# Kernel tuning notes

Hardware: AMD Instinct MI355X
Metric: run time of the kernel (lower is better)

## Reference

```python
import jax, jax.numpy as jnp
import numpy as np

B, T, F, H = 1024, 100, 64, 256


def _unif(key, shape, stdv):
    return jax.random.uniform(key, shape, jnp.float32, -stdv, stdv)


def setup_inputs() -> dict:
    key = jax.random.key(0)
    ks = jax.random.split(key, 20)
    X = jax.random.normal(ks[0], (B, T, F), jnp.float32)
    missing_mask = jnp.round(jax.random.uniform(ks[1], (B, T, F), jnp.float32))
    deltas = jax.random.uniform(ks[2], (B, T, F), jnp.float32)
    s_h = 1.0 / np.sqrt(H)
    s_f = 1.0 / np.sqrt(F)
    return {
        "X": X, "missing_mask": missing_mask, "deltas": deltas,
        # TemporalDecay h: W [H,F], b [H] (stdv = 1/sqrt(out=H))
        "W_dh": _unif(ks[3], (H, F), s_h), "b_dh": _unif(ks[4], (H,), s_h),
        # TemporalDecay x (diag): W [F,F], b [F]
        "W_dx": _unif(ks[5], (F, F), s_f), "b_dx": _unif(ks[6], (F,), s_f),
        # hist_reg: Linear(H -> F)
        "W_hist": _unif(ks[7], (F, H), s_h), "b_hist": _unif(ks[8], (F,), s_h),
        # feat_reg: W [F,F] masked by (1 - I), b [F]
        "W_feat": _unif(ks[9], (F, F), s_f), "b_feat": _unif(ks[10], (F,), s_f),
        # weight_combine: Linear(2F -> F)
        "W_comb": _unif(ks[11], (F, 2 * F), 1.0 / np.sqrt(2 * F)),
        "b_comb": _unif(ks[12], (F,), 1.0 / np.sqrt(2 * F)),
        # LSTMCell(2F -> H): gates order i,f,g,o
        "W_ih": _unif(ks[13], (4 * H, 2 * F), s_h), "b_ih": _unif(ks[14], (4 * H,), s_h),
        "W_hh": _unif(ks[15], (4 * H, H), s_h), "b_hh": _unif(ks[16], (4 * H,), s_h),
    }


def _masked_mae(inp, tgt, mask):
    return jnp.sum(jnp.abs(inp - tgt) * mask) / (jnp.sum(mask) + 1e-9)


def _rits(X, missing_mask, deltas, W_dh, b_dh, W_dx, b_dx, W_hist, b_hist,
          W_feat, b_feat, W_comb, b_comb, W_ih, b_ih, W_hh, b_hh):
    f = X.shape[-1]
    w_dx_diag = jnp.diag(W_dx)                       # diag TemporalDecay: W * eye
    W_feat_m = W_feat * (1.0 - jnp.eye(f, dtype=W_feat.dtype))

    def step(carry, xt):
        h, c, rec_loss, rec_mae = carry
        x, m, d = xt                                  # each [B, F]
        gamma_h = jnp.exp(-jax.nn.relu(d @ W_dh.T + b_dh))   # [B, H]
        gamma_x = jnp.exp(-jax.nn.relu(d * w_dx_diag + b_dx))  # [B, F]
        h = h * gamma_h
        x_h = h @ W_hist.T + b_hist
        rec_loss = rec_loss + _masked_mae(x_h, x, m)
        x_c = m * x + (1.0 - m) * x_h
        z_h = x_c @ W_feat_m.T + b_feat
        rec_loss = rec_loss + _masked_mae(z_h, x, m)
        alpha = jax.nn.sigmoid(jnp.concatenate([gamma_x, m], axis=1) @ W_comb.T + b_comb)
        c_h = alpha * z_h + (1.0 - alpha) * x_h
        rec_mae = rec_mae + _masked_mae(c_h, x, m)
        rec_loss = rec_loss + rec_mae                 # faithful to source (cumulative MAE added)
        c_c = m * x + (1.0 - m) * c_h
        inputs = jnp.concatenate([c_c, m], axis=1)    # [B, 2F]
        gates = inputs @ W_ih.T + b_ih + h @ W_hh.T + b_hh
        i_g, f_g, g_g, o_g = jnp.split(gates, 4, axis=1)
        c = jax.nn.sigmoid(f_g) * c + jax.nn.sigmoid(i_g) * jnp.tanh(g_g)
        h = jax.nn.sigmoid(o_g) * jnp.tanh(c)
        return (h, c, rec_loss, rec_mae), c_h

    b = X.shape[0]
    hsz = W_hh.shape[1]
    init = (jnp.zeros((b, hsz), X.dtype), jnp.zeros((b, hsz), X.dtype),
            jnp.asarray(0.0, X.dtype), jnp.asarray(0.0, X.dtype))
    xs = (jnp.swapaxes(X, 0, 1), jnp.swapaxes(missing_mask, 0, 1), jnp.swapaxes(deltas, 0, 1))
    (h, c, rec_loss, rec_mae), ests = jax.lax.scan(step, init, xs)
    estimations = jnp.swapaxes(ests, 0, 1)            # [B, T, F]
    imputed = missing_mask * X + (1.0 - missing_mask) * estimations
    seq_len = X.shape[1]
    return imputed, rec_mae / seq_len, rec_loss / (seq_len * 3)


def reference(X, missing_mask, deltas, W_dh, b_dh, W_dx, b_dx, W_hist, b_hist,
              W_feat, b_feat, W_comb, b_comb, W_ih, b_ih, W_hh, b_hh):
    return _rits(X, missing_mask, deltas, W_dh, b_dh, W_dx, b_dx, W_hist, b_hist,
                 W_feat, b_feat, W_comb, b_comb, W_ih, b_ih, W_hh, b_hh)
```

## Files before the change

kernel.cpp:

```cpp
#include <hip/hip_runtime.h>
#include <hip/hip_bf16.h>


#define Bz 1024
#define Tz 100
#define Fz 64
#define Hz 256
#define GROUPS 64
#define SIBS 4
#define RPB 16

typedef __attribute__((ext_vector_type(8))) short short8;
typedef __attribute__((ext_vector_type(4))) float floatx4;
typedef __hip_bfloat16 bf16;
typedef unsigned long long u64;

#define MFMA16(a, b, c) __builtin_amdgcn_mfma_f32_16x16x32_bf16((a), (b), (c), 0, 0, 0)

__device__ __forceinline__ float sigmf(float x) { return 1.0f / (1.0f + __expf(-x)); }
__device__ __forceinline__ float tanhfast(float x) { return 2.0f / (1.0f + __expf(-2.0f * x)) - 1.0f; }


__global__ void rits_convert(const float* __restrict__ Wdh, const float* __restrict__ Wdx,
                             const float* __restrict__ Whist, const float* __restrict__ Wfeat,
                             const float* __restrict__ Wcomb, const float* __restrict__ Wih,
                             const float* __restrict__ Whh, bf16* __restrict__ wsbf,
                             float* __restrict__ wdxd, unsigned int* __restrict__ flagsArr) {
    int idx = blockIdx.x * blockDim.x + threadIdx.x;
    if (idx < 4096) flagsArr[idx] = 0u;
    if (idx < 64) wdxd[idx] = Wdx[idx * 65];
    if (idx >= 438272) return;
    float v;
    if (idx < 16384) v = Wdh[idx];
    else if (idx < 32768) v = Whist[idx - 16384];
    else if (idx < 36864) { int i = idx - 32768; v = ((i >> 6) == (i & 63)) ? 0.0f : Wfeat[i]; }
    else if (idx < 45056) v = Wcomb[idx - 36864];
    else {
        int i = idx - 45056;
        int e = i & 7, q = (i >> 3) & 3, l = (i >> 5) & 15, g = (i >> 9) & 3, w = (i >> 11) & 15;
        int s = i >> 15;
        int n = g * 256 + w * 16 + l;
        v = (s < 4) ? Wih[n * 128 + s * 32 + q * 8 + e] : Whh[n * 256 + (s - 4) * 32 + q * 8 + e];
    }
    wsbf[idx] = __float2bfloat16(v);
}

__global__ __launch_bounds__(1024, 4) void rits_main(
    const float* __restrict__ X, const float* __restrict__ Mm, const float* __restrict__ Dd,
    const float* __restrict__ b_dh, const float* __restrict__ b_dx,
    const float* __restrict__ b_hist, const float* __restrict__ b_feat,
    const float* __restrict__ b_comb, const float* __restrict__ b_ih,
    const float* __restrict__ b_hh,
    const bf16* __restrict__ Wdh, const bf16* __restrict__ Whist,
    const bf16* __restrict__ Wfeatm, const bf16* __restrict__ Wcomb,
    const bf16* __restrict__ Wp5,
    const float* __restrict__ wdxd, float* __restrict__ lossbuf,
    unsigned int* __restrict__ flags, u64* __restrict__ pub, float* __restrict__ out) {
    __shared__ __align__(16) bf16 lw_hist[64 * 264];
    __shared__ __align__(16) bf16 lw_comb[64 * 136];
    __shared__ __align__(16) bf16 lw_feat[64 * 72];
    __shared__ __align__(16) bf16 lw_dh[64 * 72];
    __shared__ __align__(16) bf16 sh_hbf[RPB * 264];
    __shared__ __align__(16) float sh_x[RPB * 64];
    __shared__ __align__(16) float sh_m[RPB * 64];
    __shared__ __align__(16) bf16 sh_dbf2[RPB * 72];
    __shared__ __align__(16) bf16 sh_xcbf[RPB * 72];
    __shared__ __align__(16) bf16 sh_gmbf[RPB * 136];
    __shared__ __align__(16) bf16 sh_inbf[RPB * 136];
    __shared__ __align__(16) float sh_alpha[RPB * 68];
    __shared__ __align__(16) float sh_gam[RPB * 68];
    __shared__ __align__(16) float sh_g[4 * 16 * 66];
    __shared__ __align__(16) float sh_c[64 * 16];
    __shared__ float sh_lred[16];
    __shared__ float sh_msum[16];

    const int tid = threadIdx.x;
    const int lane = tid & 63;
    const int wid = tid >> 6;
    const int l16 = lane & 15;
    const int q = lane >> 4;
    const int j = blockIdx.x & 3;
    const int grp = blockIdx.x >> 2;
    const int b0 = grp * RPB;

    for (int i = tid; i < 64 * 256; i += 1024) lw_hist[(i >> 8) * 264 + (i & 255)] = Whist[i];
    for (int i = tid; i < 64 * 128; i += 1024) lw_comb[(i >> 7) * 136 + (i & 127)] = Wcomb[i];
    for (int i = tid; i < 64 * 64; i += 1024) {
        lw_feat[(i >> 6) * 72 + (i & 63)] = Wfeatm[i];
        lw_dh[(i >> 6) * 72 + (i & 63)] = Wdh[(j * 64 + (i >> 6)) * 64 + (i & 63)];
    }
    for (int i = tid; i < 64 * 16; i += 1024) sh_c[i] = 0.0f;
    for (int i = tid; i < RPB * 264; i += 1024) sh_hbf[i] = (bf16)0.0f;

    const int gate = wid >> 2;
    const int ct = wid & 3;
    const int nrow = gate * 256 + j * 64 + ct * 16 + l16;
    short8 wfrag[12];
#pragma unroll
    for (int s = 0; s < 12; ++s)
        wfrag[s] = *(const short8*)(Wp5 + (size_t)s * 32768 + (j * 4 + ct) * 2048 + gate * 512 +
                                    l16 * 32 + q * 8);
    const float bgate = b_ih[nrow] + b_hh[nrow];

    const float wdxf = wdxd[lane];
    const float bdxf = b_dx[lane];
    const int ca = wid * 16 + l16;
    const int colF = (wid - 4) * 16 + l16;
    const int colg = (wid - 8) * 16 + l16;
    float bc2 = 0.f, bhl = 0.f, bft = 0.f, bdl = 0.f;
    if (wid < 4) bc2 = b_comb[ca];
    else if (wid < 8) { bhl = b_hist[colF]; bft = b_feat[colF]; }
    else if (wid < 12) bdl = b_dh[j * 64 + colg];

    const size_t g0 = (size_t)(b0 + wid) * Tz * Fz + lane;
    float xv = X[g0], mv = Mm[g0], dv = Dd[g0];

    __syncthreads();

    for (int t = 0; t < Tz; ++t) {
        const bool lossStep = ((t & 3) == j);

        u64 vh = 0;
        int rc = 0, rqq = 0;
        if (t > 0 && tid >= 256) {
            int idx = tid - 256;
            int sidx = idx >> 8;
            int sib = sidx + (sidx >= j);
            rc = sib * 64 + ((idx >> 2) & 63);
            rqq = idx & 3;
            const u64* pubt = pub + ((size_t)grp * 2 + (t & 1)) * 1024;
            vh = __hip_atomic_load(pubt + (size_t)rc * 4 + rqq, __ATOMIC_RELAXED,
                                   __HIP_MEMORY_SCOPE_AGENT);
        }
        {
            const int row = wid, f = lane;
            sh_x[row * 64 + f] = xv;
            sh_m[row * 64 + f] = mv;
            float gx = __expf(-fmaxf(dv * wdxf + bdxf, 0.0f));
            sh_gmbf[row * 136 + f] = __float2bfloat16(gx);
            bf16 mb = __float2bfloat16(mv);
            sh_gmbf[row * 136 + 64 + f] = mb;
            sh_inbf[row * 136 + 64 + f] = mb;
            if (lossStep) {
                float v0 = mv;
#pragma unroll
                for (int off = 32; off; off >>= 1) v0 += __shfl_xor(v0, off, 64);
                if (lane == 0) sh_msum[wid] = v0;
            }
        }
        if (t + 1 < Tz) {
            size_t g = g0 + (size_t)(t + 1) * Fz;
            xv = X[g]; mv = Mm[g]; dv = Dd[g];
        }
        if (t > 0 && tid >= 256) {
            unsigned short* hb = (unsigned short*)sh_hbf;
#pragma unroll
            for (int r = 0; r < 4; ++r)
                hb[(rqq * 4 + r) * 264 + rc] = (unsigned short)(vh >> (16 * r));
        }
        __syncthreads();

        floatx4 acc5 = {0.f, 0.f, 0.f, 0.f};
        float xh[4];
        float l1 = 0.f, l2 = 0.f, l3 = 0.f;
        if (wid >= 4 && wid < 8) {
            floatx4 acc = {0.f, 0.f, 0.f, 0.f};
#pragma unroll
            for (int kb = 0; kb < 8; ++kb) {
                short8 a = *(const short8*)(sh_hbf + l16 * 264 + kb * 32 + q * 8);
                short8 b = *(const short8*)(lw_hist + colF * 264 + kb * 32 + q * 8);
                acc = MFMA16(a, b, acc);
            }
#pragma unroll
            for (int r = 0; r < 4; ++r) {
                int row = q * 4 + r;
                xh[r] = acc[r] + bhl;
                float xx = sh_x[row * 64 + colF], mm = sh_m[row * 64 + colF];
                l1 += fabsf(xh[r] - xx) * mm;
                float xc = mm * xx + (1.0f - mm) * xh[r];
                sh_xcbf[row * 72 + colF] = __float2bfloat16(xc);
            }
        } else {
            if (wid < 4) {
                floatx4 acca = {0.f, 0.f, 0.f, 0.f};
#pragma unroll
                for (int kb = 0; kb < 4; ++kb) {
                    short8 a = *(const short8*)(sh_gmbf + l16 * 136 + kb * 32 + q * 8);
                    short8 b = *(const short8*)(lw_comb + ca * 136 + kb * 32 + q * 8);
                    acca = MFMA16(a, b, acca);
                }
#pragma unroll
                for (int r = 0; r < 4; ++r) sh_alpha[(q * 4 + r) * 68 + ca] = sigmf(acca[r] + bc2);
            }
#pragma unroll
            for (int s = 2; s < 4; ++s) {
                short8 a = *(const short8*)(sh_inbf + l16 * 136 + s * 32 + q * 8);
                acc5 = MFMA16(a, wfrag[s], acc5);
            }
#pragma unroll
            for (int s = 4; s < 12; ++s) {
                short8 a = *(const short8*)(sh_hbf + l16 * 264 + (s - 4) * 32 + q * 8);
                acc5 = MFMA16(a, wfrag[s], acc5);
            }
        }
        if (t + 1 < Tz) sh_dbf2[wid * 72 + lane] = __float2bfloat16(dv);
        __syncthreads();

        if (wid >= 4 && wid < 8) {
            floatx4 accz = {0.f, 0.f, 0.f, 0.f};
            {
                short8 a = *(const short8*)(sh_xcbf + l16 * 72 + q * 8);
                accz = MFMA16(a, *(const short8*)(lw_feat + colF * 72 + q * 8), accz);
                a = *(const short8*)(sh_xcbf + l16 * 72 + 32 + q * 8);
                accz = MFMA16(a, *(const short8*)(lw_feat + colF * 72 + 32 + q * 8), accz);
            }
#pragma unroll
            for (int r = 0; r < 4; ++r) {
                int row = q * 4 + r;
                float xx = sh_x[row * 64 + colF], mm = sh_m[row * 64 + colF];
                float z = accz[r] + bft;
                l2 += fabsf(z - xx) * mm;
                float al = sh_alpha[row * 68 + colF];
                float ch = al * z + (1.0f - al) * xh[r];
                l3 += fabsf(ch - xx) * mm;
                float imp = mm * xx + (1.0f - mm) * ch;
                if (wid - 4 == j) out[((size_t)(b0 + row) * Tz + t) * Fz + colF] = imp;
                sh_inbf[row * 136 + colF] = __float2bfloat16(imp);
            }
            if (lossStep) {
                float v1 = l1, v2 = l2, v3 = l3;
#pragma unroll
                for (int off = 32; off; off >>= 1) {
                    v1 += __shfl_xor(v1, off, 64);
                    v2 += __shfl_xor(v2, off, 64);
                    v3 += __shfl_xor(v3, off, 64);
                }
                if (lane == 0) {
                    sh_lred[(wid - 4) * 4 + 0] = v1;
                    sh_lred[(wid - 4) * 4 + 1] = v2;
                    sh_lred[(wid - 4) * 4 + 2] = v3;
                }
            }
        } else if (wid >= 8 && wid < 12 && t + 1 < Tz) {
            short8 a0 = *(const short8*)(sh_dbf2 + l16 * 72 + q * 8);
            short8 a1 = *(const short8*)(sh_dbf2 + l16 * 72 + 32 + q * 8);
            short8 w0 = *(const short8*)(lw_dh + colg * 72 + q * 8);
            short8 w1 = *(const short8*)(lw_dh + colg * 72 + 32 + q * 8);
            floatx4 acc = {0.f, 0.f, 0.f, 0.f};
            acc = MFMA16(a0, w0, acc);
            acc = MFMA16(a1, w1, acc);
#pragma unroll
            for (int r = 0; r < 4; ++r)
                sh_gam[(q * 4 + r) * 68 + colg] = __expf(-fmaxf(acc[r] + bdl, 0.0f));
        }
        __syncthreads();

        {
#pragma unroll
            for (int s = 0; s < 2; ++s) {
                short8 a = *(const short8*)(sh_inbf + l16 * 136 + s * 32 + q * 8);
                acc5 = MFMA16(a, wfrag[s], acc5);
            }
#pragma unroll
            for (int r = 0; r < 4; ++r) {
                float v = acc5[r] + bgate;
                float tv = (gate == 2) ? tanhfast(v) : sigmf(v);
                sh_g[(gate * 16 + q * 4 + r) * 66 + ct * 16 + l16] = tv;
            }
        }
        __syncthreads();

        if (tid < 256) {
            int col = tid >> 2, q2 = tid & 3;
            int gcol = j * 64 + col;
            float4 cv = *(float4*)(sh_c + col * 16 + q2 * 4);
            float cc[4] = {cv.x, cv.y, cv.z, cv.w};
            u64 pk = 0;
#pragma unroll
            for (int r = 0; r < 4; ++r) {
                int row = q2 * 4 + r;
                float Ig = sh_g[(0 * 16 + row) * 66 + col];
                float Fg = sh_g[(1 * 16 + row) * 66 + col];
                float Gg = sh_g[(2 * 16 + row) * 66 + col];
                float Og = sh_g[(3 * 16 + row) * 66 + col];
                float c = Fg * cc[r] + Ig * Gg;
                cc[r] = c;
                if (t + 1 < Tz) {
                    float h = Og * tanhfast(c);
                    float hd = h * sh_gam[row * 68 + col];
                    bf16 hb = __float2bfloat16(hd);
                    sh_hbf[row * 264 + gcol] = hb;
                    pk |= (u64)(*(unsigned short*)&hb) << (16 * r);
                }
            }
            *(float4*)(sh_c + col * 16 + q2 * 4) = (float4){cc[0], cc[1], cc[2], cc[3]};
            if (t + 1 < Tz) {
                u64* pubn = pub + ((size_t)grp * 2 + ((t + 1) & 1)) * 1024;
                __hip_atomic_store(pubn + (size_t)gcol * 4 + q2, pk, __ATOMIC_RELAXED,
                                   __HIP_MEMORY_SCOPE_AGENT);
                asm volatile("s_waitcnt vmcnt(0)" ::: "memory");
                if (lane == 0)
                    __hip_atomic_store(&flags[((grp * 4 + j) * 4 + wid) * 4], (unsigned)(t + 2),
                                       __ATOMIC_RELAXED, __HIP_MEMORY_SCOPE_AGENT);
            }
        } else if (tid >= 960 && tid < 972 && t + 1 < Tz) {
            int sidx = (tid - 960) >> 2;
            int sib = sidx + (sidx >= j);
            int w = tid & 3;
            const unsigned target = (unsigned)(t + 2);
            unsigned it = 0;
            while (__hip_atomic_load(&flags[((grp * 4 + sib) * 4 + w) * 4], __ATOMIC_RELAXED,
                                     __HIP_MEMORY_SCOPE_AGENT) < target) {
                __builtin_amdgcn_s_sleep(1);
                if (++it > (1u << 22)) break;
            }
        }
        if (tid == 256 && lossStep) {
            float s0 = 0.0f;
#pragma unroll
            for (int i = 0; i < 16; ++i) s0 += sh_msum[i];
            float* lb = lossbuf + ((size_t)grp * Tz + t) * 4;
            lb[0] = s0;
            lb[1] = sh_lred[0] + sh_lred[4] + sh_lred[8] + sh_lred[12];
            lb[2] = sh_lred[1] + sh_lred[5] + sh_lred[9] + sh_lred[13];
            lb[3] = sh_lred[2] + sh_lred[6] + sh_lred[10] + sh_lred[14];
        }
        __syncthreads();
    }
}

__global__ void rits_finalize(const float* __restrict__ lossbuf, float* __restrict__ out) {
    __shared__ float m1[Tz], m2[Tz], m3[Tz];
    int t = threadIdx.x;
    if (t < Tz) {
        float s0 = 0.0f, s1 = 0.0f, s2 = 0.0f, s3 = 0.0f;
        for (int g = 0; g < GROUPS; ++g) {
            const float* lb = lossbuf + ((size_t)g * Tz + t) * 4;
            s0 += lb[0]; s1 += lb[1]; s2 += lb[2]; s3 += lb[3];
        }
        float inv = 1.0f / (s0 + 1e-9f);
        m1[t] = s1 * inv; m2[t] = s2 * inv; m3[t] = s3 * inv;
    }
    __syncthreads();
    if (t == 0) {
        float rm = 0.0f, rl = 0.0f;
        for (int i = 0; i < Tz; ++i) {
            rl += m1[i]; rl += m2[i]; rm += m3[i]; rl += rm;
        }
        out[(size_t)Bz * Tz * Fz] = rm / (float)Tz;
        out[(size_t)Bz * Tz * Fz + 1] = rl / (3.0f * (float)Tz);
    }
}

extern "C" void kernel_launch(void* const* d_in, const int* in_sizes, int n_in,
                              void* d_out, int out_size, void* d_ws, size_t ws_size,
                              hipStream_t stream) {
    const float* X = (const float*)d_in[0];
    const float* Mm = (const float*)d_in[1];
    const float* Dd = (const float*)d_in[2];
    const float* Wdh = (const float*)d_in[3];
    const float* b_dh = (const float*)d_in[4];
    const float* Wdx = (const float*)d_in[5];
    const float* b_dx = (const float*)d_in[6];
    const float* Whist = (const float*)d_in[7];
    const float* b_hist = (const float*)d_in[8];
    const float* Wfeat = (const float*)d_in[9];
    const float* b_feat = (const float*)d_in[10];
    const float* Wcomb = (const float*)d_in[11];
    const float* b_comb = (const float*)d_in[12];
    const float* Wih = (const float*)d_in[13];
    const float* b_ih = (const float*)d_in[14];
    const float* Whh = (const float*)d_in[15];
    const float* b_hh = (const float*)d_in[16];
    float* out = (float*)d_out;

    bf16* wsbf = (bf16*)d_ws;
    float* wdxd = (float*)((char*)d_ws + 876544);
    float* lossbuf = (float*)((char*)d_ws + 876800);
    unsigned int* flags = (unsigned int*)((char*)d_ws + 979200);
    u64* pub = (u64*)((char*)d_ws + 995584);

    rits_convert<<<1712, 256, 0, stream>>>(Wdh, Wdx, Whist, Wfeat, Wcomb, Wih, Whh, wsbf, wdxd,
                                           flags);
    rits_main<<<GROUPS * SIBS, 1024, 0, stream>>>(
        X, Mm, Dd, b_dh, b_dx, b_hist, b_feat, b_comb, b_ih, b_hh, wsbf + 0, wsbf + 16384,
        wsbf + 32768, wsbf + 36864, wsbf + 45056, wdxd, lossbuf, flags, pub, out);
    rits_finalize<<<1, 128, 0, stream>>>(lossbuf, out);
}
```

Measured before the change: 930.0 us.

## Unroll time loop by four and stage next-step inputs on idle waves

Unrolls the recurrent time loop by four with a macro and replaces single-step prefetch with a four-step register prefetch of X, mask and deltas, issued once per block of steps. Shared-memory staging for rows 4–15 of the next step moves to waves that are idle during the LSTM cell update, and the output store is deferred to that same window. This takes global-load latency and staging work off the serial per-step path between barriers. The cost is higher register pressure from twelve prefetch registers plus the unrolled body, and more intricate ownership of shared buffers across barrier phases.

```diff
diff --git a/kernel.cpp b/kernel.cpp
--- a/kernel.cpp
+++ b/kernel.cpp
@@ -113,220 +113,266 @@
     else if (wid < 12) bdl = b_dh[j * 64 + colg];
 
     const size_t g0 = (size_t)(b0 + wid) * Tz * Fz + lane;
-    float xv = X[g0], mv = Mm[g0], dv = Dd[g0];
+
+    float sx0 = 0.f, sm0 = 0.f, sd0 = 0.f;
+    float sx1 = 0.f, sm1 = 0.f, sd1 = 0.f;
+    float sx2 = 0.f, sm2 = 0.f, sd2 = 0.f;
+    float sx3 = X[g0], sm3 = Mm[g0], sd3 = Dd[g0];
 
     __syncthreads();
 
-    for (int t = 0; t < Tz; ++t) {
-        const bool lossStep = ((t & 3) == j);
-
-        u64 vh = 0;
-        int rc = 0, rqq = 0;
-        if (t > 0 && tid >= 256) {
-            int idx = tid - 256;
-            int sidx = idx >> 8;
-            int sib = sidx + (sidx >= j);
-            rc = sib * 64 + ((idx >> 2) & 63);
-            rqq = idx & 3;
-            const u64* pubt = pub + ((size_t)grp * 2 + (t & 1)) * 1024;
-            vh = __hip_atomic_load(pubt + (size_t)rc * 4 + rqq, __ATOMIC_RELAXED,
-                                   __HIP_MEMORY_SCOPE_AGENT);
+    {
+        sh_x[wid * 64 + lane] = sx3;
+        sh_m[wid * 64 + lane] = sm3;
+        float gx = __expf(-fmaxf(sd3 * wdxf + bdxf, 0.0f));
+        sh_gmbf[wid * 136 + lane] = __float2bfloat16(gx);
+        bf16 mb = __float2bfloat16(sm3);
+        sh_gmbf[wid * 136 + 64 + lane] = mb;
+        sh_inbf[wid * 136 + 64 + lane] = mb;
+        if (j == 0) {
+            float v0 = sm3;
+#pragma unroll
+            for (int off = 32; off; off >>= 1) v0 += __shfl_xor(v0, off, 64);
+            if (lane == 0) sh_msum[wid] = v0;
         }
-        {
-            const int row = wid, f = lane;
-            sh_x[row * 64 + f] = xv;
-            sh_m[row * 64 + f] = mv;
-            float gx = __expf(-fmaxf(dv * wdxf + bdxf, 0.0f));
-            sh_gmbf[row * 136 + f] = __float2bfloat16(gx);
-            bf16 mb = __float2bfloat16(mv);
-            sh_gmbf[row * 136 + 64 + f] = mb;
-            sh_inbf[row * 136 + 64 + f] = mb;
-            if (lossStep) {
-                float v0 = mv;
-#pragma unroll
-                for (int off = 32; off; off >>= 1) v0 += __shfl_xor(v0, off, 64);
-                if (lane == 0) sh_msum[wid] = v0;
-            }
-        }
-        if (t + 1 < Tz) {
-            size_t g = g0 + (size_t)(t + 1) * Fz;
-            xv = X[g]; mv = Mm[g]; dv = Dd[g];
-        }
-        if (t > 0 && tid >= 256) {
-            unsigned short* hb = (unsigned short*)sh_hbf;
-#pragma unroll
-            for (int r = 0; r < 4; ++r)
-                hb[(rqq * 4 + r) * 264 + rc] = (unsigned short)(vh >> (16 * r));
-        }
-        __syncthreads();
-
-        floatx4 acc5 = {0.f, 0.f, 0.f, 0.f};
-        float xh[4];
-        float l1 = 0.f, l2 = 0.f, l3 = 0.f;
-        if (wid >= 4 && wid < 8) {
-            floatx4 acc = {0.f, 0.f, 0.f, 0.f};
-#pragma unroll
-            for (int kb = 0; kb < 8; ++kb) {
-                short8 a = *(const short8*)(sh_hbf + l16 * 264 + kb * 32 + q * 8);
-                short8 b = *(const short8*)(lw_hist + colF * 264 + kb * 32 + q * 8);
-                acc = MFMA16(a, b, acc);
-            }
-#pragma unroll
-            for (int r = 0; r < 4; ++r) {
-                int row = q * 4 + r;
-                xh[r] = acc[r] + bhl;
-                float xx = sh_x[row * 64 + colF], mm = sh_m[row * 64 + colF];
-                l1 += fabsf(xh[r] - xx) * mm;
-                float xc = mm * xx + (1.0f - mm) * xh[r];
-                sh_xcbf[row * 72 + colF] = __float2bfloat16(xc);
-            }
-        } else {
-            if (wid < 4) {
-                floatx4 acca = {0.f, 0.f, 0.f, 0.f};
-#pragma unroll
-                for (int kb = 0; kb < 4; ++kb) {
-                    short8 a = *(const short8*)(sh_gmbf + l16 * 136 + kb * 32 + q * 8);
-                    short8 b = *(const short8*)(lw_comb + ca * 136 + kb * 32 + q * 8);
-                    acca = MFMA16(a, b, acca);
-                }
-#pragma unroll
-                for (int r = 0; r < 4; ++r) sh_alpha[(q * 4 + r) * 68 + ca] = sigmf(acca[r] + bc2);
-            }
-#pragma unroll
-            for (int s = 2; s < 4; ++s) {
-                short8 a = *(const short8*)(sh_inbf + l16 * 136 + s * 32 + q * 8);
-                acc5 = MFMA16(a, wfrag[s], acc5);
-            }
-#pragma unroll
-            for (int s = 4; s < 12; ++s) {
-                short8 a = *(const short8*)(sh_hbf + l16 * 264 + (s - 4) * 32 + q * 8);
-                acc5 = MFMA16(a, wfrag[s], acc5);
-            }
-        }
-        if (t + 1 < Tz) sh_dbf2[wid * 72 + lane] = __float2bfloat16(dv);
-        __syncthreads();
-
-        if (wid >= 4 && wid < 8) {
-            floatx4 accz = {0.f, 0.f, 0.f, 0.f};
-            {
-                short8 a = *(const short8*)(sh_xcbf + l16 * 72 + q * 8);
-                accz = MFMA16(a, *(const short8*)(lw_feat + colF * 72 + q * 8), accz);
-                a = *(const short8*)(sh_xcbf + l16 * 72 + 32 + q * 8);
-                accz = MFMA16(a, *(const short8*)(lw_feat + colF * 72 + 32 + q * 8), accz);
-            }
-#pragma unroll
-            for (int r = 0; r < 4; ++r) {
-                int row = q * 4 + r;
-                float xx = sh_x[row * 64 + colF], mm = sh_m[row * 64 + colF];
-                float z = accz[r] + bft;
-                l2 += fabsf(z - xx) * mm;
-                float al = sh_alpha[row * 68 + colF];
-                float ch = al * z + (1.0f - al) * xh[r];
-                l3 += fabsf(ch - xx) * mm;
-                float imp = mm * xx + (1.0f - mm) * ch;
-                if (wid - 4 == j) out[((size_t)(b0 + row) * Tz + t) * Fz + colF] = imp;
-                sh_inbf[row * 136 + colF] = __float2bfloat16(imp);
-            }
-            if (lossStep) {
-                float v1 = l1, v2 = l2, v3 = l3;
-#pragma unroll
-                for (int off = 32; off; off >>= 1) {
-                    v1 += __shfl_xor(v1, off, 64);
-                    v2 += __shfl_xor(v2, off, 64);
-                    v3 += __shfl_xor(v3, off, 64);
-                }
-                if (lane == 0) {
-                    sh_lred[(wid - 4) * 4 + 0] = v1;
-                    sh_lred[(wid - 4) * 4 + 1] = v2;
-                    sh_lred[(wid - 4) * 4 + 2] = v3;
-                }
-            }
-        } else if (wid >= 8 && wid < 12 && t + 1 < Tz) {
-            short8 a0 = *(const short8*)(sh_dbf2 + l16 * 72 + q * 8);
-            short8 a1 = *(const short8*)(sh_dbf2 + l16 * 72 + 32 + q * 8);
-            short8 w0 = *(const short8*)(lw_dh + colg * 72 + q * 8);
-            short8 w1 = *(const short8*)(lw_dh + colg * 72 + 32 + q * 8);
-            floatx4 acc = {0.f, 0.f, 0.f, 0.f};
-            acc = MFMA16(a0, w0, acc);
-            acc = MFMA16(a1, w1, acc);
-#pragma unroll
-            for (int r = 0; r < 4; ++r)
-                sh_gam[(q * 4 + r) * 68 + colg] = __expf(-fmaxf(acc[r] + bdl, 0.0f));
-        }
-        __syncthreads();
-
-        {
-#pragma unroll
-            for (int s = 0; s < 2; ++s) {
-                short8 a = *(const short8*)(sh_inbf + l16 * 136 + s * 32 + q * 8);
-                acc5 = MFMA16(a, wfrag[s], acc5);
-            }
-#pragma unroll
-            for (int r = 0; r < 4; ++r) {
-                float v = acc5[r] + bgate;
-                float tv = (gate == 2) ? tanhfast(v) : sigmf(v);
-                sh_g[(gate * 16 + q * 4 + r) * 66 + ct * 16 + l16] = tv;
-            }
-        }
-        __syncthreads();
-
-        if (tid < 256) {
-            int col = tid >> 2, q2 = tid & 3;
-            int gcol = j * 64 + col;
-            float4 cv = *(float4*)(sh_c + col * 16 + q2 * 4);
-            float cc[4] = {cv.x, cv.y, cv.z, cv.w};
-            u64 pk = 0;
-#pragma unroll
-            for (int r = 0; r < 4; ++r) {
-                int row = q2 * 4 + r;
-                float Ig = sh_g[(0 * 16 + row) * 66 + col];
-                float Fg = sh_g[(1 * 16 + row) * 66 + col];
-                float Gg = sh_g[(2 * 16 + row) * 66 + col];
-                float Og = sh_g[(3 * 16 + row) * 66 + col];
-                float c = Fg * cc[r] + Ig * Gg;
-                cc[r] = c;
-                if (t + 1 < Tz) {
-                    float h = Og * tanhfast(c);
-                    float hd = h * sh_gam[row * 68 + col];
-                    bf16 hb = __float2bfloat16(hd);
-                    sh_hbf[row * 264 + gcol] = hb;
-                    pk |= (u64)(*(unsigned short*)&hb) << (16 * r);
-                }
-            }
-            *(float4*)(sh_c + col * 16 + q2 * 4) = (float4){cc[0], cc[1], cc[2], cc[3]};
-            if (t + 1 < Tz) {
-                u64* pubn = pub + ((size_t)grp * 2 + ((t + 1) & 1)) * 1024;
-                __hip_atomic_store(pubn + (size_t)gcol * 4 + q2, pk, __ATOMIC_RELAXED,
-                                   __HIP_MEMORY_SCOPE_AGENT);
-                asm volatile("s_waitcnt vmcnt(0)" ::: "memory");
-                if (lane == 0)
-                    __hip_atomic_store(&flags[((grp * 4 + j) * 4 + wid) * 4], (unsigned)(t + 2),
-                                       __ATOMIC_RELAXED, __HIP_MEMORY_SCOPE_AGENT);
-            }
-        } else if (tid >= 960 && tid < 972 && t + 1 < Tz) {
-            int sidx = (tid - 960) >> 2;
-            int sib = sidx + (sidx >= j);
-            int w = tid & 3;
-            const unsigned target = (unsigned)(t + 2);
-            unsigned it = 0;
-            while (__hip_atomic_load(&flags[((grp * 4 + sib) * 4 + w) * 4], __ATOMIC_RELAXED,
-                                     __HIP_MEMORY_SCOPE_AGENT) < target) {
-                __builtin_amdgcn_s_sleep(1);
-                if (++it > (1u << 22)) break;
-            }
-        }
-        if (tid == 256 && lossStep) {
-            float s0 = 0.0f;
-#pragma unroll
-            for (int i = 0; i < 16; ++i) s0 += sh_msum[i];
-            float* lb = lossbuf + ((size_t)grp * Tz + t) * 4;
-            lb[0] = s0;
-            lb[1] = sh_lred[0] + sh_lred[4] + sh_lred[8] + sh_lred[12];
-            lb[2] = sh_lred[1] + sh_lred[5] + sh_lred[9] + sh_lred[13];
-            lb[3] = sh_lred[2] + sh_lred[6] + sh_lred[10] + sh_lred[14];
-        }
-        __syncthreads();
-    }
+    }
+
+#define RITS_STEP(T, I, XP, MP, DP, XC, MC, DC)                                                   \
+    {                                                                                             \
+        const int t = (T);                                                                        \
+        const bool lossStep = ((I) == j);                             \
+              \
+        u64 vh = 0;                                                                               \
+        int rc = 0, rqq = 0;                                                                      \
+        if (t > 0 && tid >= 256) {                                                                \
+            int idx = tid - 256;                                                                  \
+            int sidx = idx >> 8;                                                                  \
+            int sib = sidx + (sidx >= j);                                                         \
+            rc = sib * 64 + ((idx >> 2) & 63);                                                    \
+            rqq = idx & 3;                                                                        \
+            const u64* pubt = pub + ((size_t)grp * 2 + (t & 1)) * 1024;                           \
+            vh = __hip_atomic_load(pubt + (size_t)rc * 4 + rqq, __ATOMIC_RELAXED,                 \
+                                   __HIP_MEMORY_SCOPE_AGENT);                                     \
+        }                                                                                         \
+        if (tid < 256) {            \
+            sh_x[wid * 64 + lane] = (XP);                                                         \
+            sh_m[wid * 64 + lane] = (MP);                                                         \
+            float gx = __expf(-fmaxf((DP) * wdxf + bdxf, 0.0f));                                  \
+            sh_gmbf[wid * 136 + lane] = __float2bfloat16(gx);                                     \
+            bf16 mb = __float2bfloat16((MP));                                                     \
+            sh_gmbf[wid * 136 + 64 + lane] = mb;                                                  \
+            sh_inbf[wid * 136 + 64 + lane] = mb;                                                  \
+            if (lossStep) {                                                                       \
+                float v0 = (MP);                                                                  \
+                _Pragma("unroll") for (int off = 32; off; off >>= 1) v0 +=                        \
+                    __shfl_xor(v0, off, 64);                                                      \
+                if (lane == 0) sh_msum[wid] = v0;                                                 \
+            }                                                                                     \
+        }                                                                                         \
+        if ((I) == 0) {                              \
+            if (t + 1 < Tz) { size_t g = g0 + (size_t)(t + 1) * Fz; sx0 = X[g]; sm0 = Mm[g];      \
+                              sd0 = Dd[g]; }                                                      \
+            if (t + 2 < Tz) { size_t g = g0 + (size_t)(t + 2) * Fz; sx1 = X[g]; sm1 = Mm[g];      \
+                              sd1 = Dd[g]; }                                                      \
+            if (t + 3 < Tz) { size_t g = g0 + (size_t)(t + 3) * Fz; sx2 = X[g]; sm2 = Mm[g];      \
+                              sd2 = Dd[g]; }                                                      \
+            if (t + 4 < Tz) { size_t g = g0 + (size_t)(t + 4) * Fz; sx3 = X[g]; sm3 = Mm[g];      \
+                              sd3 = Dd[g]; }                                                      \
+        }                                                                                         \
+        if (t > 0 && tid >= 256) {                                                                \
+            unsigned short* hb = (unsigned short*)sh_hbf;                                         \
+            _Pragma("unroll") for (int r = 0; r < 4; ++r) hb[(rqq * 4 + r) * 264 + rc] =          \
+                (unsigned short)(vh >> (16 * r));                                                 \
+        }                                                                                         \
+        __syncthreads();                                                                \
+                                                                                \
+        floatx4 acc5 = {0.f, 0.f, 0.f, 0.f};                                                      \
+        float xh[4];                                                                              \
+        float impr[4] = {0.f, 0.f, 0.f, 0.f};                                                     \
+        float l1 = 0.f, l2 = 0.f, l3 = 0.f;                                                       \
+        if (wid >= 4 && wid < 8) {                                                                \
+            floatx4 acc = {0.f, 0.f, 0.f, 0.f};                                                   \
+            _Pragma("unroll") for (int kb = 0; kb < 8; ++kb) {                                    \
+                short8 a = *(const short8*)(sh_hbf + l16 * 264 + kb * 32 + q * 8);                \
+                short8 b = *(const short8*)(lw_hist + colF * 264 + kb * 32 + q * 8);              \
+                acc = MFMA16(a, b, acc);                                                          \
+            }                                                                                     \
+            _Pragma("unroll") for (int r = 0; r < 4; ++r) {                                       \
+                int row = q * 4 + r;                                                              \
+                xh[r] = acc[r] + bhl;                                                             \
+                float xx = sh_x[row * 64 + colF], mm = sh_m[row * 64 + colF];                     \
+                l1 += fabsf(xh[r] - xx) * mm;                                                     \
+                float xc = mm * xx + (1.0f - mm) * xh[r];                                         \
+                sh_xcbf[row * 72 + colF] = __float2bfloat16(xc);                                  \
+            }                                                                                     \
+        } else {                                                                                  \
+            if (wid < 4) {                                                                        \
+                floatx4 acca = {0.f, 0.f, 0.f, 0.f};                                              \
+                _Pragma("unroll") for (int kb = 0; kb < 4; ++kb) {                                \
+                    short8 a = *(const short8*)(sh_gmbf + l16 * 136 + kb * 32 + q * 8);           \
+                    short8 b = *(const short8*)(lw_comb + ca * 136 + kb * 32 + q * 8);            \
+                    acca = MFMA16(a, b, acca);                                                    \
+                }                                                                                 \
+                _Pragma("unroll") for (int r = 0; r < 4; ++r)                                     \
+                    sh_alpha[(q * 4 + r) * 68 + ca] = sigmf(acca[r] + bc2);                       \
+            }                                                                                     \
+            _Pragma("unroll") for (int s = 2; s < 4; ++s) {                                       \
+                short8 a = *(const short8*)(sh_inbf + l16 * 136 + s * 32 + q * 8);                \
+                acc5 = MFMA16(a, wfrag[s], acc5);                                                 \
+            }                                                                                     \
+            _Pragma("unroll") for (int s = 4; s < 12; ++s) {                                      \
+                short8 a = *(const short8*)(sh_hbf + l16 * 264 + (s - 4) * 32 + q * 8);           \
+                acc5 = MFMA16(a, wfrag[s], acc5);                                                 \
+            }                                                                                     \
+        }                                                                                         \
+        if (t + 1 < Tz) sh_dbf2[wid * 72 + lane] = __float2bfloat16((DC));                        \
+        __syncthreads();                                                                \
+                                                                                \
+        if (wid >= 4 && wid < 8) {                                                                \
+            floatx4 accz = {0.f, 0.f, 0.f, 0.f};                                                  \
+            {                                                                                     \
+                short8 a = *(const short8*)(sh_xcbf + l16 * 72 + q * 8);                          \
+                accz = MFMA16(a, *(const short8*)(lw_feat + colF * 72 + q * 8), accz);            \
+                a = *(const short8*)(sh_xcbf + l16 * 72 + 32 + q * 8);                            \
+                accz = MFMA16(a, *(const short8*)(lw_feat + colF * 72 + 32 + q * 8), accz);       \
+            }                                                                                     \
+            _Pragma("unroll") for (int r = 0; r < 4; ++r) {                                       \
+                int row = q * 4 + r;                                                              \
+                float xx = sh_x[row * 64 + colF], mm = sh_m[row * 64 + colF];                     \
+                float z = accz[r] + bft;                                                          \
+                l2 += fabsf(z - xx) * mm;                                                         \
+                float al = sh_alpha[row * 68 + colF];                                             \
+                float ch = al * z + (1.0f - al) * xh[r];                                          \
+                l3 += fabsf(ch - xx) * mm;                                                       \
+                float imp = mm * xx + (1.0f - mm) * ch;                               \
+                impr[r] = imp;                                        \
+                sh_inbf[row * 136 + colF] = __float2bfloat16(imp);                                \
+            }                                                                                     \
+            if (lossStep) {                                                                       \
+                float v1 = l1, v2 = l2, v3 = l3;                                                  \
+                _Pragma("unroll") for (int off = 32; off; off >>= 1) {                            \
+                    v1 += __shfl_xor(v1, off, 64);                                                \
+                    v2 += __shfl_xor(v2, off, 64);                                                \
+                    v3 += __shfl_xor(v3, off, 64);                                                \
+                }                                                                                 \
+                if (lane == 0) {                                                                  \
+                    sh_lred[(wid - 4) * 4 + 0] = v1;                                              \
+                    sh_lred[(wid - 4) * 4 + 1] = v2;                                              \
+                    sh_lred[(wid - 4) * 4 + 2] = v3;                                              \
+                }                                                                                 \
+            }                                                                                     \
+        } else if (wid >= 8 && wid < 12 && t + 1 < Tz) {                                          \
+            short8 a0 = *(const short8*)(sh_dbf2 + l16 * 72 + q * 8);                             \
+            short8 a1 = *(const short8*)(sh_dbf2 + l16 * 72 + 32 + q * 8);                        \
+            short8 w0 = *(const short8*)(lw_dh + colg * 72 + q * 8);                              \
+            short8 w1 = *(const short8*)(lw_dh + colg * 72 + 32 + q * 8);                         \
+            floatx4 acc = {0.f, 0.f, 0.f, 0.f};                                                   \
+            acc = MFMA16(a0, w0, acc);                                                            \
+            acc = MFMA16(a1, w1, acc);                                                            \
+            _Pragma("unroll") for (int r = 0; r < 4; ++r)                                         \
+                sh_gam[(q * 4 + r) * 68 + colg] = __expf(-fmaxf(acc[r] + bdl, 0.0f));             \
+        }                                                                                         \
+        __syncthreads();                                                                \
+                                                                                \
+        {                                                                                         \
+            _Pragma("unroll") for (int s = 0; s < 2; ++s) {                                       \
+                short8 a = *(const short8*)(sh_inbf + l16 * 136 + s * 32 + q * 8);                \
+                acc5 = MFMA16(a, wfrag[s], acc5);                                                 \
+            }                                                                                     \
+            _Pragma("unroll") for (int r = 0; r < 4; ++r) {                                       \
+                float v = acc5[r] + bgate;                                                        \
+                float tv = (gate == 2) ? tanhfast(v) : sigmf(v);                                  \
+                sh_g[(gate * 16 + q * 4 + r) * 66 + ct * 16 + l16] = tv;                          \
+            }                                                                                     \
+        }                                                                                         \
+        __syncthreads();                                                                \
+                                                             \
+        if (tid < 256) {                                                                          \
+            int col = tid >> 2, q2 = tid & 3;                                                     \
+            int gcol = j * 64 + col;                                                              \
+            float4 cv = *(float4*)(sh_c + col * 16 + q2 * 4);                                     \
+            float cc[4] = {cv.x, cv.y, cv.z, cv.w};                                               \
+            u64 pk = 0;                                                                           \
+            _Pragma("unroll") for (int r = 0; r < 4; ++r) {                                       \
+                int row = q2 * 4 + r;                                                             \
+                float Ig = sh_g[(0 * 16 + row) * 66 + col];                                       \
+                float Fg = sh_g[(1 * 16 + row) * 66 + col];                                       \
+                float Gg = sh_g[(2 * 16 + row) * 66 + col];                                       \
+                float Og = sh_g[(3 * 16 + row) * 66 + col];                                       \
+                float c = Fg * cc[r] + Ig * Gg;                                                   \
+                cc[r] = c;                                                                        \
+                if (t + 1 < Tz) {                                                                 \
+                    float h = Og * tanhfast(c);                                                   \
+                    float hd = h * sh_gam[row * 68 + col];                                        \
+                    bf16 hb = __float2bfloat16(hd);                                               \
+                    sh_hbf[row * 264 + gcol] = hb;                                                \
+                    pk |= (u64)(*(unsigned short*)&hb) << (16 * r);                               \
+                }                                                                                 \
+            }                                                                                     \
+            *(float4*)(sh_c + col * 16 + q2 * 4) = (float4){cc[0], cc[1], cc[2], cc[3]};          \
+            if (t + 1 < Tz) {                                                                     \
+                u64* pubn = pub + ((size_t)grp * 2 + ((t + 1) & 1)) * 1024;                       \
+                __hip_atomic_store(pubn + (size_t)gcol * 4 + q2, pk, __ATOMIC_RELAXED,            \
+                                   __HIP_MEMORY_SCOPE_AGENT);                                     \
+                asm volatile("s_waitcnt vmcnt(0)" ::: "memory");                                  \
+                if (lane == 0)                                                                    \
+                    __hip_atomic_store(&flags[((grp * 4 + j) * 4 + wid) * 4],                     \
+                                       (unsigned)(t + 2), __ATOMIC_RELAXED,                       \
+                                       __HIP_MEMORY_SCOPE_AGENT);                                 \
+            }                                                                                     \
+        }                                                                                         \
+        if (tid >= 256) {                                                                         \
+            if (t + 1 < Tz) {                                 \
+                sh_x[wid * 64 + lane] = (XC);                                                     \
+                sh_m[wid * 64 + lane] = (MC);                                                     \
+                float gx = __expf(-fmaxf((DC) * wdxf + bdxf, 0.0f));                              \
+                sh_gmbf[wid * 136 + lane] = __float2bfloat16(gx);                                 \
+                bf16 mb = __float2bfloat16((MC));                                                 \
+                sh_gmbf[wid * 136 + 64 + lane] = mb;                                              \
+                sh_inbf[wid * 136 + 64 + lane] = mb;                                              \
+                if ((((I) + 1) & 3) == j) {                                                       \
+                    float v0 = (MC);                                                              \
+                    _Pragma("unroll") for (int off = 32; off; off >>= 1) v0 +=                    \
+                        __shfl_xor(v0, off, 64);                                                  \
+                    if (lane == 0) sh_msum[wid] = v0;                                             \
+                }                                                                                 \
+            }                                                                                     \
+            if (wid == j + 4) {                   \
+                _Pragma("unroll") for (int r = 0; r < 4; ++r)                                     \
+                    out[((size_t)(b0 + q * 4 + r) * Tz + t) * Fz + colF] = impr[r];               \
+            }                                                                                     \
+            if (tid >= 960 && tid < 972 && t + 1 < Tz) {            \
+                int sidx = (tid - 960) >> 2;                                                      \
+                int sib = sidx + (sidx >= j);                                                     \
+                int w = tid & 3;                                                                  \
+                const unsigned target = (unsigned)(t + 2);                                        \
+                unsigned it = 0;                                                                  \
+                while (__hip_atomic_load(&flags[((grp * 4 + sib) * 4 + w) * 4],                   \
+                                         __ATOMIC_RELAXED, __HIP_MEMORY_SCOPE_AGENT) < target) {  \
+                    __builtin_amdgcn_s_sleep(1);                                                  \
+                    if (++it > (1u << 22)) break;                            \
+                }                                                                                 \
+            }                                                                                     \
+        }                                                                                         \
+        if (tid == 256 && lossStep) {                                                             \
+            float s0 = 0.0f;                                                                      \
+            _Pragma("unroll") for (int i = 0; i < 16; ++i) s0 += sh_msum[i];                      \
+            float* lb = lossbuf + ((size_t)grp * Tz + t) * 4;                                     \
+            lb[0] = s0;                                                                           \
+            lb[1] = sh_lred[0] + sh_lred[4] + sh_lred[8] + sh_lred[12];                           \
+            lb[2] = sh_lred[1] + sh_lred[5] + sh_lred[9] + sh_lred[13];                           \
+            lb[3] = sh_lred[2] + sh_lred[6] + sh_lred[10] + sh_lred[14];                          \
+        }                                                                                         \
+        __syncthreads();                                                                \
+    }
+
+    for (int tb = 0; tb < Tz; tb += 4) {
+        RITS_STEP(tb + 0, 0, sx3, sm3, sd3, sx0, sm0, sd0)
+        RITS_STEP(tb + 1, 1, sx0, sm0, sd0, sx1, sm1, sd1)
+        RITS_STEP(tb + 2, 2, sx1, sm1, sd1, sx2, sm2, sd2)
+        RITS_STEP(tb + 3, 3, sx2, sm2, sd2, sx3, sm3, sd3)
+    }
+#undef RITS_STEP
 }
 
 __global__ void rits_finalize(const float* __restrict__ lossbuf, float* __restrict__ out) {
```

Measured after the change: 1.120 ms. 1.2x slower.
